# Kernel optimization log

Measured on AMD Instinct MI355X. Metric: run time of the kernel, lower is better.

The kernel has to match this reference:

```python
import jax, jax.numpy as jnp
import numpy as np

GFD = 4096   # global feature dim (VGG fc7)
DH = 1024    # 2 * hidden_dim


def setup_inputs() -> dict:
    key = jax.random.key(0)
    ks = jax.random.split(key, 10)
    b, t_k = 32, 196
    s = lambda fan_in: 1.0 / np.sqrt(fan_in)
    return {
        "global_features": jax.random.normal(ks[0], (b, t_k, GFD), jnp.float32),
        "s_t_hat": jax.random.normal(ks[1], (b, DH), jnp.float32),
        "coverage_img": jnp.zeros((b, t_k, 1), jnp.float32),
        # params
        "Wg": jax.random.normal(ks[2], (GFD, GFD), jnp.float32) * s(GFD),
        "bg": jnp.zeros((GFD,), jnp.float32),
        "Gs": jax.random.normal(ks[3], (GFD, DH), jnp.float32) * s(GFD),
        "bgs": jnp.zeros((DH,), jnp.float32),
        "Wgs": jax.random.normal(ks[4], (DH, DH), jnp.float32) * s(DH),  # w_g_star, no bias
        "Wdec": jax.random.normal(ks[5], (DH, DH), jnp.float32) * s(DH),  # decode_proj
        "bdec": jnp.zeros((DH,), jnp.float32),
        "v": jax.random.normal(ks[6], (DH, 1), jnp.float32) * s(DH),  # score vector, no bias
    }


def reference(global_features, s_t_hat, coverage_img, Wg, bg, Gs, bgs, Wgs, Wdec, bdec, v):
    # g_star: project 4096-d region features -> 1024-d   [b, t_k, DH]
    g1 = global_features @ Wg + bg
    g_star = g1 @ Gs + bgs
    # additive (Bahdanau) scores with coverage
    w_g_star = g_star @ Wgs                       # [b, t_k, DH]
    dec_fea = s_t_hat @ Wdec + bdec               # [b, DH]
    e_a = jnp.tanh(w_g_star + dec_fea[:, None, :] + coverage_img)  # [b, t_k, DH]
    scores = e_a @ v                              # [b, t_k, 1]
    alpha_a = jax.nn.softmax(scores, axis=1)      # softmax over regions
    # attention-weighted context (the bmm)
    c_img = jnp.einsum("bt,btd->bd", alpha_a[..., 0], g_star)  # [b, DH]
    coverage_new = coverage_img + alpha_a
    return c_img, coverage_new, alpha_a
```

## Files before the change

kernel.cpp:

```cpp
#include <hip/hip_runtime.h>
#include <hip/hip_bf16.h>

typedef __attribute__((ext_vector_type(8))) short short8;
typedef __attribute__((ext_vector_type(4))) float floatx4;

#define GLOBAL_AS __attribute__((address_space(1)))
#define LDS_AS    __attribute__((address_space(3)))

__device__ __forceinline__ unsigned short f2bf_rne(float x) {
  unsigned int u = __float_as_uint(x);
  u += 0x7fffu + ((u >> 16) & 1u);
  return (unsigned short)(u >> 16);
}

__device__ __forceinline__ void cast8_body(const float* __restrict__ in,
                                           unsigned short* __restrict__ out,
                                           int blk, int n8) {
  int i = blk * 256 + threadIdx.x;
  if (i >= n8) return;
  const float4* p = (const float4*)in;
  float4 v0 = p[2 * i], v1 = p[2 * i + 1];
  short8 o;
  o[0] = (short)f2bf_rne(v0.x); o[1] = (short)f2bf_rne(v0.y);
  o[2] = (short)f2bf_rne(v0.z); o[3] = (short)f2bf_rne(v0.w);
  o[4] = (short)f2bf_rne(v1.x); o[5] = (short)f2bf_rne(v1.y);
  o[6] = (short)f2bf_rne(v1.z); o[7] = (short)f2bf_rne(v1.w);
  *(short8*)(out + 8 * (size_t)i) = o;
}

__device__ __forceinline__ void trans32_body(const float* __restrict__ in,
                                             unsigned short* __restrict__ out,
                                             int R, int C, int bx, int by) {
  __shared__ unsigned short tile[32][33];
  int tx = threadIdx.x & 31, ty = threadIdx.x >> 5;
  int r0 = by * 32, c0 = bx * 32;
#pragma unroll
  for (int j = 0; j < 32; j += 8)
    tile[ty + j][tx] = f2bf_rne(in[(size_t)(r0 + ty + j) * C + c0 + tx]);
  __syncthreads();
#pragma unroll
  for (int j = 0; j < 32; j += 8)
    out[(size_t)(c0 + ty + j) * R + r0 + tx] = tile[tx][ty + j];
}

__global__ void prep1_kernel(const float* __restrict__ gf, unsigned short* __restrict__ gf_bf,
                             const float* __restrict__ Wg, unsigned short* __restrict__ Wg_bf,
                             const float* __restrict__ Gs, unsigned short* __restrict__ GsT,
                             const float* __restrict__ bg, float* __restrict__ bias1,
                             const float* __restrict__ Wgs, unsigned short* __restrict__ WgsT,
                             const float* __restrict__ bdec, float* __restrict__ dec,
                             float* __restrict__ scores) {
  const int b = blockIdx.x;
  if (b < 12544) {
    cast8_body(gf, gf_bf, b, 3211264);
  } else if (b < 20736) {
    cast8_body(Wg, Wg_bf, b - 12544, 2097152);
  } else if (b < 24832) {
    int bb = b - 20736;
    trans32_body(Gs, GsT, 4096, 1024, bb & 31, bb >> 5);
  } else if (b < 24896) {
    int bb = b - 24832;
    int j = (bb & 3) * 256 + threadIdx.x;
    int k0 = (bb >> 2) * 256;
    float acc = 0.f;
    for (int k = 0; k < 256; ++k) acc += bg[k0 + k] * Gs[(size_t)(k0 + k) * 1024 + j];
    atomicAdd(&bias1[j], acc);
  } else if (b < 25920) {
    int bb = b - 24896;
    trans32_body(Wgs, WgsT, 1024, 1024, bb & 31, bb >> 5);
  } else if (b < 26048) {
    int i = (b - 25920) * 256 + threadIdx.x;
    dec[i] = bdec[i & 1023];
  } else {
    int i = (b - 26048) * 256 + threadIdx.x;
    if (i < 1568) ((float4*)scores)[i] = make_float4(0.f, 0.f, 0.f, 0.f);
  }
}

__global__ void dec_accum_kernel(const float* __restrict__ sth, const float* __restrict__ Wdec,
                                 float* __restrict__ dec) {
  __shared__ float ss[32][128];
  const int tid = threadIdx.x;
  const int k0 = blockIdx.y * 128;
  for (int i = tid; i < 32 * 128; i += 256) {
    int bb = i >> 7, kk = i & 127;
    ss[bb][kk] = sth[bb * 1024 + k0 + kk];
  }
  __syncthreads();
  const int j = blockIdx.x * 256 + tid;
  float acc[32];
#pragma unroll
  for (int b = 0; b < 32; ++b) acc[b] = 0.f;
  for (int kk = 0; kk < 128; ++kk) {
    float w = Wdec[(size_t)(k0 + kk) * 1024 + j];
#pragma unroll
    for (int b = 0; b < 32; ++b) acc[b] += ss[b][kk] * w;
  }
  for (int b = 0; b < 32; ++b) atomicAdd(&dec[b * 1024 + j], acc[b]);
}

template <int BM, int BN, bool HAS_BIAS, bool WRITE_F32, bool WRITE_BF16, bool SWAPXY>
__global__ __launch_bounds__(256, 4) void gemm_tile_kernel(
    const unsigned short* __restrict__ A, const unsigned short* __restrict__ BT,
    const float* __restrict__ bias, float* __restrict__ Cf,
    unsigned short* __restrict__ Cb, int M, int N, int K) {
  constexpr int AF = BM / 32;
  constexpr int BF = BN / 32;
  constexpr int ASLAB = BM * 64;
  constexpr int BSLAB = BN * 64;
  __shared__ unsigned short lds_a[BM * 64];
  __shared__ unsigned short lds_b[BN * 64];
  const int tid = threadIdx.x;
  const int lane = tid & 63;
  const int wave = tid >> 6;
  const int wm = wave >> 1, wn = wave & 1;
  const int quad = lane >> 4, col = lane & 15;

  const int gx = (int)gridDim.x;
  const int nwg = gx * (int)gridDim.y;
  const int bid = (int)blockIdx.y * gx + (int)blockIdx.x;
  const int swz = (bid & 7) * (nwg >> 3) + (bid >> 3);
  const int bx = swz % gx, by = swz / gx;
  const int m0 = (SWAPXY ? bx : by) * BM;
  const int n0 = (SWAPXY ? by : bx) * BN;

  floatx4 acc[AF][BF] = {};

  const int srow = tid >> 2;
  const int skoff = ((tid & 3) ^ ((tid >> 3) & 3)) * 8;
  const unsigned short* a_ptr = A + (size_t)(m0 + srow) * K + skoff;
  const unsigned short* b_ptr = BT + (size_t)(n0 + srow) * K + skoff;
  const size_t rowskip = (size_t)64 * K;
  char* const la_dst = (char*)lds_a + tid * 16;
  char* const lb_dst = (char*)lds_b + tid * 16;
  const int cx = (quad ^ ((col >> 1) & 3)) * 16;

  for (int kt = 0; kt < K; kt += 64) {
    __syncthreads();
#pragma unroll
    for (int h = 0; h < BM / 64; ++h)
#pragma unroll
      for (int s = 0; s < 2; ++s)
        __builtin_amdgcn_global_load_lds((const GLOBAL_AS void*)(a_ptr + h * rowskip + s * 32),
                                         (LDS_AS void*)(la_dst + s * ASLAB + h * 4096), 16, 0, 0);
#pragma unroll
    for (int h = 0; h < BN / 64; ++h)
#pragma unroll
      for (int s = 0; s < 2; ++s)
        __builtin_amdgcn_global_load_lds((const GLOBAL_AS void*)(b_ptr + h * rowskip + s * 32),
                                         (LDS_AS void*)(lb_dst + s * BSLAB + h * 4096), 16, 0, 0);
    a_ptr += 64; b_ptr += 64;
    __syncthreads();
#pragma unroll
    for (int s = 0; s < 2; ++s) {
      short8 af[AF], bf[BF];
#pragma unroll
      for (int tf = 0; tf < AF; ++tf)
        af[tf] = *(const short8*)((const char*)lds_a + s * ASLAB +
                                  (wm * (BM / 2) + tf * 16 + col) * 64 + cx);
#pragma unroll
      for (int tf = 0; tf < BF; ++tf)
        bf[tf] = *(const short8*)((const char*)lds_b + s * BSLAB +
                                  (wn * (BN / 2) + tf * 16 + col) * 64 + cx);
#pragma unroll
      for (int tm = 0; tm < AF; ++tm)
#pragma unroll
        for (int tn = 0; tn < BF; ++tn)
          acc[tm][tn] = __builtin_amdgcn_mfma_f32_16x16x32_bf16(af[tm], bf[tn], acc[tm][tn], 0, 0, 0);
    }
  }

#pragma unroll
  for (int tm = 0; tm < AF; ++tm) {
    const int mg = m0 + wm * (BM / 2) + tm * 16 + quad * 4;
#pragma unroll
    for (int tn = 0; tn < BF; ++tn) {
      const int ng = n0 + wn * (BN / 2) + tn * 16 + col;
      const float bv = HAS_BIAS ? bias[ng] : 0.0f;
#pragma unroll
      for (int r = 0; r < 4; ++r) {
        const float val = acc[tm][tn][r] + bv;
        if (WRITE_F32) Cf[(size_t)(mg + r) * N + ng] = val;
        if (WRITE_BF16) Cb[(size_t)(mg + r) * N + ng] = f2bf_rne(val);
      }
    }
  }
}

__global__ __launch_bounds__(256, 4) void gemm_scores_kernel(
    const unsigned short* __restrict__ A, const unsigned short* __restrict__ BT,
    const float* __restrict__ dec, const float* __restrict__ cov,
    const float* __restrict__ v, float* __restrict__ scores, int M, int N, int K) {
  constexpr int ASLAB = 8192;
  constexpr int BSLAB = 4096;
  __shared__ unsigned short lds_a[128 * 64];
  __shared__ unsigned short lds_b[64 * 64];
  const int tid = threadIdx.x;
  const int lane = tid & 63;
  const int wave = tid >> 6;
  const int wm = wave >> 1, wn = wave & 1;
  const int quad = lane >> 4, col = lane & 15;

  const int gx = (int)gridDim.x;
  const int nwg = gx * (int)gridDim.y;
  const int bid = (int)blockIdx.y * gx + (int)blockIdx.x;
  const int swz = (bid & 7) * (nwg >> 3) + (bid >> 3);
  const int m0 = (swz / gx) * 128, n0 = (swz % gx) * 64;

  floatx4 acc[4][2] = {};

  const int srow = tid >> 2;
  const int skoff = ((tid & 3) ^ ((tid >> 3) & 3)) * 8;
  const unsigned short* a_ptr = A + (size_t)(m0 + srow) * K + skoff;
  const unsigned short* b_ptr = BT + (size_t)(n0 + srow) * K + skoff;
  const size_t rowskip = (size_t)64 * K;
  char* const la_dst = (char*)lds_a + tid * 16;
  char* const lb_dst = (char*)lds_b + tid * 16;
  const int cx = (quad ^ ((col >> 1) & 3)) * 16;

  for (int kt = 0; kt < K; kt += 64) {
    __syncthreads();
#pragma unroll
    for (int h = 0; h < 2; ++h)
#pragma unroll
      for (int s = 0; s < 2; ++s)
        __builtin_amdgcn_global_load_lds((const GLOBAL_AS void*)(a_ptr + h * rowskip + s * 32),
                                         (LDS_AS void*)(la_dst + s * ASLAB + h * 4096), 16, 0, 0);
#pragma unroll
    for (int s = 0; s < 2; ++s)
      __builtin_amdgcn_global_load_lds((const GLOBAL_AS void*)(b_ptr + s * 32),
                                       (LDS_AS void*)(lb_dst + s * BSLAB), 16, 0, 0);
    a_ptr += 64; b_ptr += 64;
    __syncthreads();
#pragma unroll
    for (int s = 0; s < 2; ++s) {
      short8 af[4], bf[2];
#pragma unroll
      for (int tf = 0; tf < 4; ++tf)
        af[tf] = *(const short8*)((const char*)lds_a + s * ASLAB +
                                  (wm * 64 + tf * 16 + col) * 64 + cx);
#pragma unroll
      for (int tf = 0; tf < 2; ++tf)
        bf[tf] = *(const short8*)((const char*)lds_b + s * BSLAB +
                                  (wn * 32 + tf * 16 + col) * 64 + cx);
#pragma unroll
      for (int tm = 0; tm < 4; ++tm)
#pragma unroll
        for (int tn = 0; tn < 2; ++tn)
          acc[tm][tn] = __builtin_amdgcn_mfma_f32_16x16x32_bf16(af[tm], bf[tn], acc[tm][tn], 0, 0, 0);
    }
  }

  const int n_base = n0 + wn * 32;
  float vv[2];
#pragma unroll
  for (int tn = 0; tn < 2; ++tn) vv[tn] = v[n_base + tn * 16 + col];
#pragma unroll
  for (int tm = 0; tm < 4; ++tm) {
#pragma unroll
    for (int r = 0; r < 4; ++r) {
      const int row = m0 + wm * 64 + tm * 16 + quad * 4 + r;
      const int b = row / 196;
      const float cw = cov[row];
      const float* dr = dec + b * 1024 + n_base;
      float s = 0.f;
#pragma unroll
      for (int tn = 0; tn < 2; ++tn)
        s += tanhf(acc[tm][tn][r] + dr[tn * 16 + col] + cw) * vv[tn];
      s += __shfl_xor(s, 1, 64);
      s += __shfl_xor(s, 2, 64);
      s += __shfl_xor(s, 4, 64);
      s += __shfl_xor(s, 8, 64);
      if ((lane & 15) == 0) atomicAdd(&scores[row], s);
    }
  }
}

__global__ void softmax_kernel(const float* __restrict__ scores, const float* __restrict__ cov,
                               float* __restrict__ alpha_ws, float* __restrict__ out) {
  const int b = blockIdx.x, tid = threadIdx.x;
  const int lane = tid & 63, wid = tid >> 6;
  __shared__ float red[8];
  float s = (tid < 196) ? scores[b * 196 + tid] : -1e30f;
  float m = s;
  for (int off = 32; off > 0; off >>= 1) m = fmaxf(m, __shfl_xor(m, off, 64));
  if (lane == 0) red[wid] = m;
  __syncthreads();
  m = fmaxf(fmaxf(red[0], red[1]), fmaxf(red[2], red[3]));
  float e = (tid < 196) ? __expf(s - m) : 0.f;
  float t = e;
  for (int off = 32; off > 0; off >>= 1) t += __shfl_xor(t, off, 64);
  if (lane == 0) red[4 + wid] = t;
  __syncthreads();
  const float tot = red[4] + red[5] + red[6] + red[7];
  const float a = e / tot;
  if (tid < 196) {
    alpha_ws[b * 196 + tid] = a;
    out[32768 + b * 196 + tid] = cov[b * 196 + tid] + a;
    out[32768 + 6272 + b * 196 + tid] = a;
  }
}

__global__ __launch_bounds__(256) void ctx_kernel(const float* __restrict__ alpha,
                                                  const float* __restrict__ gstar,
                                                  float* __restrict__ out) {
  const int b = blockIdx.y;
  const int colbase = blockIdx.x * 128;
  const int c = threadIdx.x & 127;
  const int half = threadIdx.x >> 7;
  const float* g = gstar + ((size_t)b * 196 + half * 98) * 1024 + colbase + c;
  const float* al = alpha + b * 196 + half * 98;
  float acc = 0.f;
#pragma unroll 7
  for (int t = 0; t < 98; ++t) acc += al[t] * g[(size_t)t * 1024];
  __shared__ float part[256];
  part[threadIdx.x] = acc;
  __syncthreads();
  if (threadIdx.x < 128)
    out[b * 1024 + colbase + threadIdx.x] = part[threadIdx.x] + part[threadIdx.x + 128];
}

extern "C" void kernel_launch(void* const* d_in, const int* in_sizes, int n_in,
                              void* d_out, int out_size, void* d_ws, size_t ws_size,
                              hipStream_t stream) {
  (void)in_sizes; (void)n_in; (void)out_size; (void)ws_size;
  const float* gf   = (const float*)d_in[0];
  const float* sth  = (const float*)d_in[1];
  const float* cov  = (const float*)d_in[2];
  const float* Wg   = (const float*)d_in[3];
  const float* bg   = (const float*)d_in[4];
  const float* Gs   = (const float*)d_in[5];
  const float* bgs  = (const float*)d_in[6];
  const float* Wgs  = (const float*)d_in[7];
  const float* Wdec = (const float*)d_in[8];
  const float* bdec = (const float*)d_in[9];
  const float* v    = (const float*)d_in[10];
  float* out = (float*)d_out;

  char* ws = (char*)d_ws;
  unsigned short* gf_bf   = (unsigned short*)(ws + 0);
  unsigned short* Wg_bf   = (unsigned short*)(ws + 51380224);
  float*          gstar_f = (float*)(ws + 51380224);
  unsigned short* GsT     = (unsigned short*)(ws + 84934656);
  unsigned short* gstar_b = (unsigned short*)(ws + 84934656);
  unsigned short* C1T_b   = (unsigned short*)(ws + 102760448);
  unsigned short* WgsT    = (unsigned short*)(ws + 111149056);
  float*          bias1   = (float*)(ws + 113246208);
  float*          dec     = (float*)(ws + 113262592);
  float*          scores  = (float*)(ws + 113393664);
  float*          alpha   = (float*)(ws + 113426432);

  hipMemcpyAsync(bias1, bgs, 4096, hipMemcpyDeviceToDevice, stream);
  prep1_kernel<<<26055, 256, 0, stream>>>(gf, gf_bf, Wg, Wg_bf, Gs, GsT, bg, bias1,
                                          Wgs, WgsT, bdec, dec, scores);
  dec_accum_kernel<<<dim3(4, 8), 256, 0, stream>>>(sth, Wdec, dec);
  gemm_tile_kernel<128, 64, false, false, true, true><<<dim3(8, 64), 256, 0, stream>>>(
      GsT, Wg_bf, nullptr, nullptr, C1T_b, 1024, 4096, 4096);
  gemm_tile_kernel<128, 128, true, true, true, false><<<dim3(8, 49), 256, 0, stream>>>(
      gf_bf, C1T_b, bias1, gstar_f, gstar_b, 6272, 1024, 4096);
  gemm_scores_kernel<<<dim3(16, 49), 256, 0, stream>>>(
      gstar_b, WgsT, dec, cov, v, scores, 6272, 1024, 1024);
  softmax_kernel<<<32, 256, 0, stream>>>(scores, cov, alpha, out);
  ctx_kernel<<<dim3(8, 32), 256, 0, stream>>>(alpha, gstar_f, out);
}
```

Measured before the change: 478.9 us.

## Fuse fp32-to-bf16 casts into GEMM operand loads and merge dec projection into gemm1

The separate passes that converted global_features and Wg to bf16 in a workspace are removed. Both GEMMs now read the fp32 operand into registers, convert it, and write it to LDS, with the next tile prefetched in registers while the current one is computed. The decode projection blocks are folded into the gemm1 launch as extra blocks. This drops a full write and re-read of roughly 77 MB of bf16 copies and one launch, at the cost of more register pressure (launch bounds lowered to 2) and synchronous fp32 loads in place of async global-to-LDS copies for one operand.

```diff
diff --git a/kernel.cpp b/kernel.cpp
--- a/kernel.cpp
+++ b/kernel.cpp
@@ -11,21 +11,6 @@
   unsigned int u = __float_as_uint(x);
   u += 0x7fffu + ((u >> 16) & 1u);
   return (unsigned short)(u >> 16);
-}
-
-__device__ __forceinline__ void cast8_body(const float* __restrict__ in,
-                                           unsigned short* __restrict__ out,
-                                           int blk, int n8) {
-  int i = blk * 256 + threadIdx.x;
-  if (i >= n8) return;
-  const float4* p = (const float4*)in;
-  float4 v0 = p[2 * i], v1 = p[2 * i + 1];
-  short8 o;
-  o[0] = (short)f2bf_rne(v0.x); o[1] = (short)f2bf_rne(v0.y);
-  o[2] = (short)f2bf_rne(v0.z); o[3] = (short)f2bf_rne(v0.w);
-  o[4] = (short)f2bf_rne(v1.x); o[5] = (short)f2bf_rne(v1.y);
-  o[6] = (short)f2bf_rne(v1.z); o[7] = (short)f2bf_rne(v1.w);
-  *(short8*)(out + 8 * (size_t)i) = o;
 }
 
 __device__ __forceinline__ void trans32_body(const float* __restrict__ in,
@@ -43,76 +28,171 @@
     out[(size_t)(c0 + ty + j) * R + r0 + tx] = tile[tx][ty + j];
 }
 
-__global__ void prep1_kernel(const float* __restrict__ gf, unsigned short* __restrict__ gf_bf,
-                             const float* __restrict__ Wg, unsigned short* __restrict__ Wg_bf,
-                             const float* __restrict__ Gs, unsigned short* __restrict__ GsT,
+__global__ void prep0_kernel(const float* __restrict__ Gs, unsigned short* __restrict__ GsT,
+                             const float* __restrict__ Wgs, unsigned short* __restrict__ WgsT,
                              const float* __restrict__ bg, float* __restrict__ bias1,
-                             const float* __restrict__ Wgs, unsigned short* __restrict__ WgsT,
                              const float* __restrict__ bdec, float* __restrict__ dec,
                              float* __restrict__ scores) {
   const int b = blockIdx.x;
-  if (b < 12544) {
-    cast8_body(gf, gf_bf, b, 3211264);
-  } else if (b < 20736) {
-    cast8_body(Wg, Wg_bf, b - 12544, 2097152);
-  } else if (b < 24832) {
-    int bb = b - 20736;
-    trans32_body(Gs, GsT, 4096, 1024, bb & 31, bb >> 5);
-  } else if (b < 24896) {
-    int bb = b - 24832;
+  if (b < 4096) {
+    trans32_body(Gs, GsT, 4096, 1024, b & 31, b >> 5);
+  } else if (b < 5120) {
+    int bb = b - 4096;
+    trans32_body(Wgs, WgsT, 1024, 1024, bb & 31, bb >> 5);
+  } else if (b < 5184) {
+    int bb = b - 5120;
     int j = (bb & 3) * 256 + threadIdx.x;
     int k0 = (bb >> 2) * 256;
     float acc = 0.f;
     for (int k = 0; k < 256; ++k) acc += bg[k0 + k] * Gs[(size_t)(k0 + k) * 1024 + j];
     atomicAdd(&bias1[j], acc);
-  } else if (b < 25920) {
-    int bb = b - 24896;
-    trans32_body(Wgs, WgsT, 1024, 1024, bb & 31, bb >> 5);
-  } else if (b < 26048) {
-    int i = (b - 25920) * 256 + threadIdx.x;
+  } else if (b < 5312) {
+    int i = (b - 5184) * 256 + threadIdx.x;
     dec[i] = bdec[i & 1023];
   } else {
-    int i = (b - 26048) * 256 + threadIdx.x;
+    int i = (b - 5312) * 256 + threadIdx.x;
     if (i < 1568) ((float4*)scores)[i] = make_float4(0.f, 0.f, 0.f, 0.f);
   }
 }
 
-__global__ void dec_accum_kernel(const float* __restrict__ sth, const float* __restrict__ Wdec,
-                                 float* __restrict__ dec) {
-  __shared__ float ss[32][128];
+__global__ __launch_bounds__(256, 2) void gemm1_kernel(
+    const unsigned short* __restrict__ A, const float* __restrict__ Bw,
+    unsigned short* __restrict__ Cb,
+    const float* __restrict__ sth, const float* __restrict__ Wdec,
+    float* __restrict__ dec) {
+  constexpr int K = 4096, NT = 64;
+  constexpr int ASLAB = 8192, BSLAB = 4096;
+  __shared__ unsigned short lds_a[128 * 64];
+  __shared__ unsigned short lds_b[64 * 64];
   const int tid = threadIdx.x;
-  const int k0 = blockIdx.y * 128;
-  for (int i = tid; i < 32 * 128; i += 256) {
-    int bb = i >> 7, kk = i & 127;
-    ss[bb][kk] = sth[bb * 1024 + k0 + kk];
-  }
-  __syncthreads();
-  const int j = blockIdx.x * 256 + tid;
-  float acc[32];
-#pragma unroll
-  for (int b = 0; b < 32; ++b) acc[b] = 0.f;
-  for (int kk = 0; kk < 128; ++kk) {
-    float w = Wdec[(size_t)(k0 + kk) * 1024 + j];
-#pragma unroll
-    for (int b = 0; b < 32; ++b) acc[b] += ss[b][kk] * w;
-  }
-  for (int b = 0; b < 32; ++b) atomicAdd(&dec[b * 1024 + j], acc[b]);
-}
-
-template <int BM, int BN, bool HAS_BIAS, bool WRITE_F32, bool WRITE_BF16, bool SWAPXY>
-__global__ __launch_bounds__(256, 4) void gemm_tile_kernel(
-    const unsigned short* __restrict__ A, const unsigned short* __restrict__ BT,
+  const int bid = (int)blockIdx.x;
+
+  if (bid >= 512) {
+    float* ss = (float*)lds_a;
+    const int db = bid - 512;
+    const int k0 = (db >> 2) * 128;
+    for (int i = tid; i < 32 * 128; i += 256) {
+      int bb = i >> 7, kk = i & 127;
+      ss[bb * 128 + kk] = sth[bb * 1024 + k0 + kk];
+    }
+    __syncthreads();
+    const int j = (db & 3) * 256 + tid;
+    float acc2[32];
+#pragma unroll
+    for (int b = 0; b < 32; ++b) acc2[b] = 0.f;
+    for (int kk = 0; kk < 128; ++kk) {
+      float w = Wdec[(size_t)(k0 + kk) * 1024 + j];
+#pragma unroll
+      for (int b = 0; b < 32; ++b) acc2[b] += ss[b * 128 + kk] * w;
+    }
+    for (int b = 0; b < 32; ++b) atomicAdd(&dec[b * 1024 + j], acc2[b]);
+    return;
+  }
+
+  const int lane = tid & 63, wave = tid >> 6;
+  const int wm = wave >> 1, wn = wave & 1;
+  const int quad = lane >> 4, col = lane & 15;
+  const int swz = (bid & 7) * 64 + (bid >> 3);
+  const int m0 = (swz & 7) * 128;
+  const int n0 = (swz >> 3) * 64;
+
+  floatx4 acc[4][2] = {};
+
+  const int srow = tid >> 2;
+  const int skoff = ((tid & 3) ^ ((tid >> 3) & 3)) * 8;
+  const unsigned short* a_ptr = A + (size_t)(m0 + srow) * K + skoff;
+  const float* b_src = Bw + (size_t)(n0 + srow) * K + skoff;
+  const size_t rowskip = (size_t)64 * K;
+  char* const la_dst = (char*)lds_a + tid * 16;
+  char* const lb_dst = (char*)lds_b + tid * 16;
+  const int cx = (quad ^ ((col >> 1) & 3)) * 16;
+
+  float4 rB0[4], rB1[4];
+  auto LOADB = [&](float4* r, int t) {
+    const float* p = b_src + (size_t)t * 64;
+#pragma unroll
+    for (int s = 0; s < 2; ++s) {
+      r[2 * s]     = *(const float4*)(p + s * 32);
+      r[2 * s + 1] = *(const float4*)(p + s * 32 + 4);
+    }
+  };
+  auto WRITEB = [&](const float4* r) {
+#pragma unroll
+    for (int s = 0; s < 2; ++s) {
+      short8 o;
+      o[0] = (short)f2bf_rne(r[2 * s].x);     o[1] = (short)f2bf_rne(r[2 * s].y);
+      o[2] = (short)f2bf_rne(r[2 * s].z);     o[3] = (short)f2bf_rne(r[2 * s].w);
+      o[4] = (short)f2bf_rne(r[2 * s + 1].x); o[5] = (short)f2bf_rne(r[2 * s + 1].y);
+      o[6] = (short)f2bf_rne(r[2 * s + 1].z); o[7] = (short)f2bf_rne(r[2 * s + 1].w);
+      *(short8*)(lb_dst + s * BSLAB) = o;
+    }
+  };
+  auto STAGEA = [&](int t) {
+    const unsigned short* p = a_ptr + (size_t)t * 64;
+#pragma unroll
+    for (int h = 0; h < 2; ++h)
+#pragma unroll
+      for (int s = 0; s < 2; ++s)
+        __builtin_amdgcn_global_load_lds((const GLOBAL_AS void*)(p + h * rowskip + s * 32),
+                                         (LDS_AS void*)(la_dst + s * ASLAB + h * 4096), 16, 0, 0);
+  };
+  auto COMPUTE = [&]() {
+#pragma unroll
+    for (int s = 0; s < 2; ++s) {
+      short8 af[4], bf[2];
+#pragma unroll
+      for (int tf = 0; tf < 4; ++tf)
+        af[tf] = *(const short8*)((const char*)lds_a + s * ASLAB +
+                                  (wm * 64 + tf * 16 + col) * 64 + cx);
+#pragma unroll
+      for (int tf = 0; tf < 2; ++tf)
+        bf[tf] = *(const short8*)((const char*)lds_b + s * BSLAB +
+                                  (wn * 32 + tf * 16 + col) * 64 + cx);
+#pragma unroll
+      for (int tm = 0; tm < 4; ++tm)
+#pragma unroll
+        for (int tn = 0; tn < 2; ++tn)
+          acc[tm][tn] = __builtin_amdgcn_mfma_f32_16x16x32_bf16(af[tm], bf[tn], acc[tm][tn], 0, 0, 0);
+    }
+  };
+  auto STEP = [&](float4* cur, float4* nxt, int t, bool pf) {
+    __syncthreads();
+    STAGEA(t);
+    WRITEB(cur);
+    if (pf) LOADB(nxt, t + 1);
+    __syncthreads();
+    COMPUTE();
+  };
+
+  LOADB(rB0, 0);
+  for (int t = 0; t < NT; t += 2) {
+    STEP(rB0, rB1, t, true);
+    STEP(rB1, rB0, t + 1, t + 2 < NT);
+  }
+
+#pragma unroll
+  for (int tm = 0; tm < 4; ++tm) {
+    const int mg = m0 + wm * 64 + tm * 16 + quad * 4;
+#pragma unroll
+    for (int tn = 0; tn < 2; ++tn) {
+      const int ng = n0 + wn * 32 + tn * 16 + col;
+#pragma unroll
+      for (int r = 0; r < 4; ++r)
+        Cb[(size_t)(mg + r) * 4096 + ng] = f2bf_rne(acc[tm][tn][r]);
+    }
+  }
+}
+
+__global__ __launch_bounds__(256, 2) void gemm2_kernel(
+    const float* __restrict__ Af, const unsigned short* __restrict__ BT,
     const float* __restrict__ bias, float* __restrict__ Cf,
-    unsigned short* __restrict__ Cb, int M, int N, int K) {
-  constexpr int AF = BM / 32;
-  constexpr int BF = BN / 32;
-  constexpr int ASLAB = BM * 64;
-  constexpr int BSLAB = BN * 64;
-  __shared__ unsigned short lds_a[BM * 64];
-  __shared__ unsigned short lds_b[BN * 64];
+    unsigned short* __restrict__ Cb) {
+  constexpr int K = 4096, NT = 64, N = 1024;
+  constexpr int ASLAB = 8192, BSLAB = 8192;
+  __shared__ unsigned short lds_a[128 * 64];
+  __shared__ unsigned short lds_b[128 * 64];
   const int tid = threadIdx.x;
-  const int lane = tid & 63;
-  const int wave = tid >> 6;
+  const int lane = tid & 63, wave = tid >> 6;
   const int wm = wave >> 1, wn = wave & 1;
   const int quad = lane >> 4, col = lane & 15;
 
@@ -120,68 +200,99 @@
   const int nwg = gx * (int)gridDim.y;
   const int bid = (int)blockIdx.y * gx + (int)blockIdx.x;
   const int swz = (bid & 7) * (nwg >> 3) + (bid >> 3);
-  const int bx = swz % gx, by = swz / gx;
-  const int m0 = (SWAPXY ? bx : by) * BM;
-  const int n0 = (SWAPXY ? by : bx) * BN;
-
-  floatx4 acc[AF][BF] = {};
+  const int m0 = (swz / gx) * 128, n0 = (swz % gx) * 128;
+
+  floatx4 acc[4][4] = {};
 
   const int srow = tid >> 2;
   const int skoff = ((tid & 3) ^ ((tid >> 3) & 3)) * 8;
-  const unsigned short* a_ptr = A + (size_t)(m0 + srow) * K + skoff;
+  const float* a_src = Af + (size_t)(m0 + srow) * K + skoff;
   const unsigned short* b_ptr = BT + (size_t)(n0 + srow) * K + skoff;
   const size_t rowskip = (size_t)64 * K;
   char* const la_dst = (char*)lds_a + tid * 16;
   char* const lb_dst = (char*)lds_b + tid * 16;
   const int cx = (quad ^ ((col >> 1) & 3)) * 16;
 
-  for (int kt = 0; kt < K; kt += 64) {
-    __syncthreads();
-#pragma unroll
-    for (int h = 0; h < BM / 64; ++h)
+  float4 rA0[8], rA1[8];
+  auto LOADA = [&](float4* r, int t) {
+    const float* p = a_src + (size_t)t * 64;
+#pragma unroll
+    for (int h = 0; h < 2; ++h)
+#pragma unroll
+      for (int s = 0; s < 2; ++s) {
+        r[h * 4 + 2 * s]     = *(const float4*)(p + h * rowskip + s * 32);
+        r[h * 4 + 2 * s + 1] = *(const float4*)(p + h * rowskip + s * 32 + 4);
+      }
+  };
+  auto WRITEA = [&](const float4* r) {
+#pragma unroll
+    for (int h = 0; h < 2; ++h)
+#pragma unroll
+      for (int s = 0; s < 2; ++s) {
+        const float4 a = r[h * 4 + 2 * s], b = r[h * 4 + 2 * s + 1];
+        short8 o;
+        o[0] = (short)f2bf_rne(a.x); o[1] = (short)f2bf_rne(a.y);
+        o[2] = (short)f2bf_rne(a.z); o[3] = (short)f2bf_rne(a.w);
+        o[4] = (short)f2bf_rne(b.x); o[5] = (short)f2bf_rne(b.y);
+        o[6] = (short)f2bf_rne(b.z); o[7] = (short)f2bf_rne(b.w);
+        *(short8*)(la_dst + s * ASLAB + h * 4096) = o;
+      }
+  };
+  auto STAGEB = [&](int t) {
+    const unsigned short* p = b_ptr + (size_t)t * 64;
+#pragma unroll
+    for (int h = 0; h < 2; ++h)
 #pragma unroll
       for (int s = 0; s < 2; ++s)
-        __builtin_amdgcn_global_load_lds((const GLOBAL_AS void*)(a_ptr + h * rowskip + s * 32),
-                                         (LDS_AS void*)(la_dst + s * ASLAB + h * 4096), 16, 0, 0);
-#pragma unroll
-    for (int h = 0; h < BN / 64; ++h)
-#pragma unroll
-      for (int s = 0; s < 2; ++s)
-        __builtin_amdgcn_global_load_lds((const GLOBAL_AS void*)(b_ptr + h * rowskip + s * 32),
+        __builtin_amdgcn_global_load_lds((const GLOBAL_AS void*)(p + h * rowskip + s * 32),
                                          (LDS_AS void*)(lb_dst + s * BSLAB + h * 4096), 16, 0, 0);
-    a_ptr += 64; b_ptr += 64;
-    __syncthreads();
+  };
+  auto COMPUTE = [&]() {
 #pragma unroll
     for (int s = 0; s < 2; ++s) {
-      short8 af[AF], bf[BF];
-#pragma unroll
-      for (int tf = 0; tf < AF; ++tf)
+      short8 af[4], bf[4];
+#pragma unroll
+      for (int tf = 0; tf < 4; ++tf)
         af[tf] = *(const short8*)((const char*)lds_a + s * ASLAB +
-                                  (wm * (BM / 2) + tf * 16 + col) * 64 + cx);
-#pragma unroll
-      for (int tf = 0; tf < BF; ++tf)
+                                  (wm * 64 + tf * 16 + col) * 64 + cx);
+#pragma unroll
+      for (int tf = 0; tf < 4; ++tf)
         bf[tf] = *(const short8*)((const char*)lds_b + s * BSLAB +
-                                  (wn * (BN / 2) + tf * 16 + col) * 64 + cx);
-#pragma unroll
-      for (int tm = 0; tm < AF; ++tm)
-#pragma unroll
-        for (int tn = 0; tn < BF; ++tn)
+                                  (wn * 64 + tf * 16 + col) * 64 + cx);
+#pragma unroll
+      for (int tm = 0; tm < 4; ++tm)
+#pragma unroll
+        for (int tn = 0; tn < 4; ++tn)
           acc[tm][tn] = __builtin_amdgcn_mfma_f32_16x16x32_bf16(af[tm], bf[tn], acc[tm][tn], 0, 0, 0);
     }
-  }
-
-#pragma unroll
-  for (int tm = 0; tm < AF; ++tm) {
-    const int mg = m0 + wm * (BM / 2) + tm * 16 + quad * 4;
-#pragma unroll
-    for (int tn = 0; tn < BF; ++tn) {
-      const int ng = n0 + wn * (BN / 2) + tn * 16 + col;
-      const float bv = HAS_BIAS ? bias[ng] : 0.0f;
+  };
+  auto STEP = [&](float4* cur, float4* nxt, int t, bool pf) {
+    __syncthreads();
+    STAGEB(t);
+    WRITEA(cur);
+    if (pf) LOADA(nxt, t + 1);
+    __syncthreads();
+    COMPUTE();
+  };
+
+  LOADA(rA0, 0);
+  for (int t = 0; t < NT; t += 2) {
+    STEP(rA0, rA1, t, true);
+    STEP(rA1, rA0, t + 1, t + 2 < NT);
+  }
+
+#pragma unroll
+  for (int tm = 0; tm < 4; ++tm) {
+    const int mg = m0 + wm * 64 + tm * 16 + quad * 4;
+#pragma unroll
+    for (int tn = 0; tn < 4; ++tn) {
+      const int ng = n0 + wn * 64 + tn * 16 + col;
+      const float bv = bias[ng];
 #pragma unroll
       for (int r = 0; r < 4; ++r) {
         const float val = acc[tm][tn][r] + bv;
-        if (WRITE_F32) Cf[(size_t)(mg + r) * N + ng] = val;
-        if (WRITE_BF16) Cb[(size_t)(mg + r) * N + ng] = f2bf_rne(val);
+        Cf[(size_t)(mg + r) * N + ng] = val;
+        Cb[(size_t)(mg + r) * N + ng] = f2bf_rne(val);
       }
     }
   }
@@ -338,26 +449,20 @@
   float* out = (float*)d_out;
 
   char* ws = (char*)d_ws;
-  unsigned short* gf_bf   = (unsigned short*)(ws + 0);
-  unsigned short* Wg_bf   = (unsigned short*)(ws + 51380224);
-  float*          gstar_f = (float*)(ws + 51380224);
-  unsigned short* GsT     = (unsigned short*)(ws + 84934656);
-  unsigned short* gstar_b = (unsigned short*)(ws + 84934656);
-  unsigned short* C1T_b   = (unsigned short*)(ws + 102760448);
-  unsigned short* WgsT    = (unsigned short*)(ws + 111149056);
-  float*          bias1   = (float*)(ws + 113246208);
-  float*          dec     = (float*)(ws + 113262592);
-  float*          scores  = (float*)(ws + 113393664);
-  float*          alpha   = (float*)(ws + 113426432);
+  unsigned short* GsT     = (unsigned short*)(ws + 0);
+  unsigned short* C1T_b   = (unsigned short*)(ws + 8388608);
+  unsigned short* WgsT    = (unsigned short*)(ws + 16777216);
+  float*          gstar_f = (float*)(ws + 18874368);
+  unsigned short* gstar_b = (unsigned short*)(ws + 44564480);
+  float*          bias1   = (float*)(ws + 57409536);
+  float*          dec     = (float*)(ws + 57413632);
+  float*          scores  = (float*)(ws + 57544704);
+  float*          alpha   = (float*)(ws + 57569792);
 
   hipMemcpyAsync(bias1, bgs, 4096, hipMemcpyDeviceToDevice, stream);
-  prep1_kernel<<<26055, 256, 0, stream>>>(gf, gf_bf, Wg, Wg_bf, Gs, GsT, bg, bias1,
-                                          Wgs, WgsT, bdec, dec, scores);
-  dec_accum_kernel<<<dim3(4, 8), 256, 0, stream>>>(sth, Wdec, dec);
-  gemm_tile_kernel<128, 64, false, false, true, true><<<dim3(8, 64), 256, 0, stream>>>(
-      GsT, Wg_bf, nullptr, nullptr, C1T_b, 1024, 4096, 4096);
-  gemm_tile_kernel<128, 128, true, true, true, false><<<dim3(8, 49), 256, 0, stream>>>(
-      gf_bf, C1T_b, bias1, gstar_f, gstar_b, 6272, 1024, 4096);
+  prep0_kernel<<<5319, 256, 0, stream>>>(Gs, GsT, Wgs, WgsT, bg, bias1, bdec, dec, scores);
+  gemm1_kernel<<<544, 256, 0, stream>>>(GsT, Wg, C1T_b, sth, Wdec, dec);
+  gemm2_kernel<<<dim3(8, 49), 256, 0, stream>>>(gf, C1T_b, bias1, gstar_f, gstar_b);
   gemm_scores_kernel<<<dim3(16, 49), 256, 0, stream>>>(
       gstar_b, WgsT, dec, cov, v, scores, 6272, 1024, 1024);
   softmax_kernel<<<32, 256, 0, stream>>>(scores, cov, alpha, out);
```

After: 462.7 us. 1.03x faster.
